# Kernel tuning notes

Measured on AMD Instinct MI355X. Metric: run time of the kernel, lower is better.

The kernel has to match this reference:

```python
import jax, jax.numpy as jnp
import numpy as np

B, M = 32768, 200
NUM_LAYERS, OW, OH = 22, 11, 11
CNN_CH, HIDDEN = 128, 512
ACTION_NVEC = (9, 10)


def setup_inputs() -> dict:
    key = jax.random.key(0)
    ks = jax.random.split(key, 16)
    s = 0.02
    inp = {
        "observations": jax.random.randint(ks[0], (B, M, 3), 0, 256, dtype=jnp.int32),
        "max_vec": jnp.ones((NUM_LAYERS,), dtype=jnp.float32),
        "w_conv1": jax.random.normal(ks[1], (CNN_CH, NUM_LAYERS, 5, 5), jnp.float32) * s,
        "b_conv1": jnp.zeros((CNN_CH,), jnp.float32),
        "w_conv2": jax.random.normal(ks[2], (CNN_CH, CNN_CH, 3, 3), jnp.float32) * s,
        "b_conv2": jnp.zeros((CNN_CH,), jnp.float32),
        "w_fc": jax.random.normal(ks[3], (CNN_CH, HIDDEN // 2), jnp.float32) * s,
        "b_fc": jnp.zeros((HIDDEN // 2,), jnp.float32),
        "w_self": jax.random.normal(ks[4], (NUM_LAYERS, HIDDEN // 2), jnp.float32) * s,
        "b_self": jnp.zeros((HIDDEN // 2,), jnp.float32),
        "w_actor0": jax.random.normal(ks[5], (HIDDEN, ACTION_NVEC[0]), jnp.float32) * 0.01,
        "b_actor0": jnp.zeros((ACTION_NVEC[0],), jnp.float32),
        "w_actor1": jax.random.normal(ks[6], (HIDDEN, ACTION_NVEC[1]), jnp.float32) * 0.01,
        "b_actor1": jnp.zeros((ACTION_NVEC[1],), jnp.float32),
        "w_value": jax.random.normal(ks[7], (HIDDEN, 1), jnp.float32) * s,
        "b_value": jnp.zeros((1,), jnp.float32),
    }
    return inp


def _conv(x, w, b, stride):
    y = jax.lax.conv_general_dilated(
        x, w, window_strides=(stride, stride), padding="VALID",
        dimension_numbers=("NCHW", "OIHW", "NCHW"))
    return y + b[None, :, None, None]


def _encode(observations, max_vec, w_conv1, b_conv1, w_conv2, b_conv2,
            w_fc, b_fc, w_self, b_self):
    # torch: token_observations[token_observations == 255] = 0
    obs = jnp.where(observations == 255, 0, observations)
    coords = obs[..., 0]                       # [B, M]
    x_idx = (coords >> 4) & 15
    y_idx = coords & 15
    atr_idx = obs[..., 1]
    atr_val = obs[..., 2].astype(jnp.float32)
    # coords_byte != 255 is always True after the 255->0 rewrite above
    valid = (x_idx < OW) & (y_idx < OH) & (atr_idx < NUM_LAYERS)
    b_idx = jnp.broadcast_to(jnp.arange(obs.shape[0])[:, None], coords.shape)
    # route invalid tokens to a dummy batch slot B, then drop it
    b_idx = jnp.where(valid, b_idx, obs.shape[0])
    a_idx = jnp.where(valid, atr_idx, 0)
    xs = jnp.where(valid, x_idx, 0)
    ys = jnp.where(valid, y_idx, 0)
    box = jnp.zeros((obs.shape[0] + 1, NUM_LAYERS, OW, OH), jnp.float32)
    box = box.at[b_idx, a_idx, xs, ys].set(atr_val)[: obs.shape[0]]
    features = box / max_vec[None, :, None, None]
    self_feat = jax.nn.relu(features[:, :, 5, 5] @ w_self + b_self)   # [B, 256]
    h = jax.nn.relu(_conv(features, w_conv1, b_conv1, 3))             # [B,128,3,3]
    h = jax.nn.relu(_conv(h, w_conv2, b_conv2, 1))                    # [B,128,1,1]
    h = h.reshape(h.shape[0], -1)                                     # [B,128]
    cnn_feat = jax.nn.relu(h @ w_fc + b_fc)                           # [B,256]
    return jnp.concatenate([self_feat, cnn_feat], axis=1)             # [B,512]


def reference(observations, max_vec, w_conv1, b_conv1, w_conv2, b_conv2,
              w_fc, b_fc, w_self, b_self, w_actor0, b_actor0,
              w_actor1, b_actor1, w_value, b_value):
    hidden = _encode(observations, max_vec, w_conv1, b_conv1, w_conv2, b_conv2,
                     w_fc, b_fc, w_self, b_self)
    logits0 = hidden @ w_actor0 + b_actor0
    logits1 = hidden @ w_actor1 + b_actor1
    value = hidden @ w_value + b_value
    return (logits0, logits1, value, hidden)
```

## Files before the change

kernel.cpp:

```cpp
#include <hip/hip_runtime.h>
#include <hip/hip_bf16.h>

typedef unsigned int uint;
typedef unsigned short ushort;
typedef unsigned long long ull;
typedef __attribute__((ext_vector_type(8))) short short8;
typedef __attribute__((ext_vector_type(4))) float float4_;

#define B_TOT 32768
#define NL    22
#define HID0  ((long)B_TOT * 20)

#define W2F_OFF  0
#define WFCF_OFF 294912
#define WHF_OFF  360448
#define W1T_OFF  393216
#define H1_OFF   674816

__device__ __forceinline__ ushort f2bf(float v) {
  uint x = __float_as_uint(v);
  x += 0x7fffu + ((x >> 16) & 1u);
  return (ushort)(x >> 16);
}

extern "C" __global__ __launch_bounds__(256)
void k_prep(const float* __restrict__ wc1, const float* __restrict__ wc2,
            const float* __restrict__ wfc,
            const float* __restrict__ wa0, const float* __restrict__ wa1,
            const float* __restrict__ wv,
            ushort* __restrict__ w2f, ushort* __restrict__ wfcf,
            ushort* __restrict__ whf, float* __restrict__ w1t)
{
  int i = blockIdx.x * 256 + threadIdx.x;
  if (i < 18432) {
    int l = i & 63, cg = (i >> 6) & 7, ks = i >> 9;
    int col = cg * 16 + (l & 15), kb = ks * 32 + (l >> 4) * 8;
    ushort t[8];
    #pragma unroll
    for (int j = 0; j < 8; ++j) t[j] = f2bf(wc2[col * 1152 + kb + j]);
    uint4 o = { (uint)t[0]|((uint)t[1]<<16), (uint)t[2]|((uint)t[3]<<16),
                (uint)t[4]|((uint)t[5]<<16), (uint)t[6]|((uint)t[7]<<16) };
    ((uint4*)w2f)[i] = o;
  } else if (i < 22528) {
    int i2 = i - 18432;
    int l = i2 & 63, cg = (i2 >> 6) & 15, ks = i2 >> 10;
    int col = cg * 16 + (l & 15), kb = ks * 32 + (l >> 4) * 8;
    ushort t[8];
    #pragma unroll
    for (int j = 0; j < 8; ++j) t[j] = f2bf(wfc[(kb + j) * 256 + col]);
    uint4 o = { (uint)t[0]|((uint)t[1]<<16), (uint)t[2]|((uint)t[3]<<16),
                (uint)t[4]|((uint)t[5]<<16), (uint)t[6]|((uint)t[7]<<16) };
    ((uint4*)wfcf)[i2] = o;
  } else if (i < 24576) {
    int i2 = i - 22528;
    int l = i2 & 63, cg = (i2 >> 6) & 1, ks = i2 >> 7;
    int col = cg * 16 + (l & 15), kb = ks * 32 + (l >> 4) * 8;
    ushort t[8];
    #pragma unroll
    for (int j = 0; j < 8; ++j) {
      int k = kb + j;
      float v = (col < 9)  ? wa0[k*9 + col]
              : (col < 19) ? wa1[k*10 + (col - 9)]
              : (col == 19) ? wv[k] : 0.f;
      t[j] = f2bf(v);
    }
    uint4 o = { (uint)t[0]|((uint)t[1]<<16), (uint)t[2]|((uint)t[3]<<16),
                (uint)t[4]|((uint)t[5]<<16), (uint)t[6]|((uint)t[7]<<16) };
    ((uint4*)whf)[i2] = o;
  } else if (i < 24576 + 70400) {
    int j = i - 24576;
    int oc = j & 127, r = j >> 7;
    w1t[j] = wc1[oc * 550 + r];
  }
}

extern "C" __global__ __launch_bounds__(256)
void k_encode(const int* __restrict__ obs, const float* __restrict__ maxvec,
              const float* __restrict__ w1t, const float* __restrict__ bc1,
              const float* __restrict__ wself, const float* __restrict__ bself,
              float* __restrict__ out, ushort* __restrict__ h1g)
{
  __shared__ uint4  tksf[600];
  __shared__ uint   klist[4][64];
  __shared__ ushort h1su[4][1152];
  __shared__ float  rmaxv[NL];

  const int tid = threadIdx.x, lane = tid & 63, w = tid >> 6;
  const long b = (long)blockIdx.x * 4 + w;

  const uint4* o4 = (const uint4*)obs + (long)blockIdx.x * 600;
  for (int i = tid; i < 600; i += 256) tksf[i] = o4[i];
  if (tid < NL) rmaxv[tid] = 1.0f / maxvec[tid];
  __syncthreads();

  const uint* toks = (const uint*)&tksf[w * 150];
  int cnt = 0;
  #pragma unroll
  for (int r = 0; r < 4; ++r) {
    int m = r * 64 + lane;
    bool valid = false; uint pk = 0;
    if (m < 200) {
      int c = (int)toks[m*3], a = (int)toks[m*3+1], v = (int)toks[m*3+2];
      c = (c == 255) ? 0 : c;  a = (a == 255) ? 0 : a;  v = (v == 255) ? 0 : v;
      int x = (c >> 4) & 15, y = c & 15;
      valid = (x < 11) && (y < 11) && (a < NL);
      pk = ((uint)a << 16) | ((uint)x << 12) | ((uint)y << 8) | (uint)v;
    }
    ull bal = __ballot(valid);
    if (valid) {
      int pos = cnt + __popcll(bal & ((1ull << lane) - 1ull));
      if (pos < 64) klist[w][pos] = pk;
    }
    cnt += __popcll(bal);
  }
  if (cnt > 64) cnt = 64;

  uint u = 0; bool alive = false;
  if (lane < cnt) {
    u = klist[w][lane];
    alive = true;
    uint cell = u >> 8;
    for (int t2 = lane + 1; t2 < cnt; ++t2)
      if ((klist[w][t2] >> 8) == cell) { alive = false; break; }
  }
  ull bal2 = __ballot(alive);
  const int n2 = __popcll(bal2);
  if (alive) {
    int pos = __popcll(bal2 & ((1ull << lane) - 1ull));
    klist[w][pos] = u;
  }
  __syncthreads();

  float a0[9] = {0,0,0,0,0,0,0,0,0}, a1[9] = {0,0,0,0,0,0,0,0,0};
  float s0 = 0.f, s1 = 0.f, s2 = 0.f, s3 = 0.f;
  uint tk = klist[w][0];
  for (int t = 0; t < n2; ++t) {
    uint cur = tk;
    tk = klist[w][(t + 1) & 63];
    int a = cur >> 16, x = (cur >> 12) & 15, y = (cur >> 8) & 15;
    float fv = (float)(cur & 255u) * rmaxv[a];
    if (x == 5 && y == 5) {
      s0 = fmaf(fv, wself[a*256 + lane      ], s0);
      s1 = fmaf(fv, wself[a*256 + 64  + lane], s1);
      s2 = fmaf(fv, wself[a*256 + 128 + lane], s2);
      s3 = fmaf(fv, wself[a*256 + 192 + lane], s3);
    }
    #pragma unroll
    for (int ox = 0; ox < 3; ++ox) {
      int kx = x - 3 * ox;
      if ((unsigned)kx > 4u) continue;
      #pragma unroll
      for (int oy = 0; oy < 3; ++oy) {
        int ky = y - 3 * oy;
        if ((unsigned)ky > 4u) continue;
        const float* wr = w1t + (a*25 + kx*5 + ky) * 128;
        a0[ox*3+oy] = fmaf(fv, wr[lane],      a0[ox*3+oy]);
        a1[ox*3+oy] = fmaf(fv, wr[64 + lane], a1[ox*3+oy]);
      }
    }
  }

  out[HID0 + b*512 + lane      ] = fmaxf(s0 + bself[lane      ], 0.f);
  out[HID0 + b*512 + 64  + lane] = fmaxf(s1 + bself[64  + lane], 0.f);
  out[HID0 + b*512 + 128 + lane] = fmaxf(s2 + bself[128 + lane], 0.f);
  out[HID0 + b*512 + 192 + lane] = fmaxf(s3 + bself[192 + lane], 0.f);

  float bb0 = bc1[lane], bb1 = bc1[64 + lane];
  #pragma unroll
  for (int p = 0; p < 9; ++p) {
    h1su[w][lane*9 + p]        = f2bf(fmaxf(a0[p] + bb0, 0.f));
    h1su[w][(64 + lane)*9 + p] = f2bf(fmaxf(a1[p] + bb1, 0.f));
  }
  const uint* sv = (const uint*)&h1su[w][0];
  const int bbk = (int)(b >> 6), r = (int)(b & 63);
  uint* dstu = (uint*)h1g;
  const long cbase = ((long)bbk * 36) * 64 + r;
  #pragma unroll
  for (int i = lane; i < 576; i += 64) {
    int t = i >> 4;
    dstu[(cbase + (long)t * 64) * 16 + (i & 15)] = sv[i];
  }
}

extern "C" __global__ __launch_bounds__(256)
void k_mlp(const ushort* __restrict__ h1g, const ushort* __restrict__ w2f,
           const float* __restrict__ bc2, const ushort* __restrict__ wfcf,
           const float* __restrict__ bfc, const ushort* __restrict__ whf,
           const float* __restrict__ ba0, const float* __restrict__ ba1,
           const float* __restrict__ bv, float* __restrict__ out)
{
  __shared__ short  Abuf[2][4][64][8];
  __shared__ ushort h2A[16][64][8];

  const int tid = threadIdx.x, lane = tid & 63, w = tid >> 6;
  const int lo = lane & 15, hi = lane >> 4;
  const int bb = blockIdx.x, b0 = bb * 64;

  const short8* w2fv  = (const short8*)w2f;
  const short8* wfcfv = (const short8*)wfcf;
  const uint4*  A4    = (const uint4*)h1g + (long)bb * 36 * 256;

  float4_ acc[4][2];
  #pragma unroll
  for (int cgi = 0; cgi < 2; ++cgi) {
    float bv_ = bc2[(2*w + cgi)*16 + lo];
    float4_ t = {bv_, bv_, bv_, bv_};
    #pragma unroll
    for (int m = 0; m < 4; ++m) acc[m][cgi] = t;
  }

  uint4 rA = A4[tid];
  for (int t = 0; t < 36; ++t) {
    const int cur = t & 1;
    *(uint4*)&Abuf[cur][tid & 3][tid >> 2][0] = rA;
    if (t + 1 < 36) rA = A4[(t + 1) * 256 + tid];
    __syncthreads();
    short8 af[4];
    #pragma unroll
    for (int m = 0; m < 4; ++m)
      af[m] = *(const short8*)&Abuf[cur][hi][m*16 + lo][0];
    #pragma unroll
    for (int cgi = 0; cgi < 2; ++cgi) {
      short8 bf = w2fv[(t*8 + 2*w + cgi)*64 + lane];
      #pragma unroll
      for (int m = 0; m < 4; ++m)
        acc[m][cgi] = __builtin_amdgcn_mfma_f32_16x16x32_bf16(af[m], bf, acc[m][cgi], 0, 0, 0);
    }
  }
  __syncthreads();

  #pragma unroll
  for (int cgi = 0; cgi < 2; ++cgi) {
    int col = (2*w + cgi)*16 + lo;
    #pragma unroll
    for (int m = 0; m < 4; ++m)
      #pragma unroll
      for (int q = 0; q < 4; ++q) {
        int R = m*16 + hi*4 + q;
        h2A[col >> 3][R][col & 7] = f2bf(fmaxf(acc[m][cgi][q], 0.f));
      }
  }
  __syncthreads();

  float4_ acc2[4][4];
  #pragma unroll
  for (int cgi = 0; cgi < 4; ++cgi) {
    float bv_ = bfc[(4*w + cgi)*16 + lo];
    float4_ t = {bv_, bv_, bv_, bv_};
    #pragma unroll
    for (int m = 0; m < 4; ++m) acc2[m][cgi] = t;
  }
  #pragma unroll
  for (int ks = 0; ks < 4; ++ks) {
    short8 af[4];
    #pragma unroll
    for (int m = 0; m < 4; ++m)
      af[m] = *(const short8*)&h2A[ks*4 + hi][m*16 + lo][0];
    #pragma unroll
    for (int cgi = 0; cgi < 4; ++cgi) {
      short8 bf = wfcfv[(ks*16 + 4*w + cgi)*64 + lane];
      #pragma unroll
      for (int m = 0; m < 4; ++m)
        acc2[m][cgi] = __builtin_amdgcn_mfma_f32_16x16x32_bf16(af[m], bf, acc2[m][cgi], 0, 0, 0);
    }
  }

  #pragma unroll
  for (int cgi = 0; cgi < 4; ++cgi) {
    int col = (4*w + cgi)*16 + lo;
    #pragma unroll
    for (int m = 0; m < 4; ++m)
      #pragma unroll
      for (int q = 0; q < 4; ++q) {
        int R = m*16 + hi*4 + q;
        out[HID0 + (long)(b0 + R)*512 + 256 + col] = fmaxf(acc2[m][cgi][q], 0.f);
      }
  }
  __syncthreads();

  const short8* whfv = (const short8*)whf;
  float4_ acc3[2];
  #pragma unroll
  for (int cg = 0; cg < 2; ++cg) {
    int col = cg*16 + lo;
    float bias = (col < 9) ? ba0[col] : (col < 19) ? ba1[col - 9]
               : (col == 19) ? bv[0] : 0.f;
    float4_ t = {bias, bias, bias, bias};
    acc3[cg] = t;
  }

  const float* hrow = out + HID0 + (long)(b0 + w*16 + lo) * 512;
  #pragma unroll
  for (int ks = 0; ks < 16; ++ks) {
    float4_ f0 = *(const float4_*)(hrow + ks*32 + hi*8);
    float4_ f1 = *(const float4_*)(hrow + ks*32 + hi*8 + 4);
    union { short8 s; ushort u[8]; } afu;
    afu.u[0] = f2bf(f0[0]); afu.u[1] = f2bf(f0[1]);
    afu.u[2] = f2bf(f0[2]); afu.u[3] = f2bf(f0[3]);
    afu.u[4] = f2bf(f1[0]); afu.u[5] = f2bf(f1[1]);
    afu.u[6] = f2bf(f1[2]); afu.u[7] = f2bf(f1[3]);
    #pragma unroll
    for (int cg = 0; cg < 2; ++cg) {
      short8 bf = whfv[(ks*2 + cg)*64 + lane];
      acc3[cg] = __builtin_amdgcn_mfma_f32_16x16x32_bf16(afu.s, bf, acc3[cg], 0, 0, 0);
    }
  }

  #pragma unroll
  for (int cg = 0; cg < 2; ++cg) {
    int col = cg*16 + lo;
    #pragma unroll
    for (int q = 0; q < 4; ++q) {
      long R = b0 + w*16 + hi*4 + q;
      float v = acc3[cg][q];
      if (col < 9)        out[R*9 + col] = v;
      else if (col < 19)  out[(long)B_TOT*9 + R*10 + (col - 9)] = v;
      else if (col == 19) out[(long)B_TOT*19 + R] = v;
    }
  }
}

extern "C" void kernel_launch(void* const* d_in, const int* in_sizes, int n_in,
                              void* d_out, int out_size, void* d_ws, size_t ws_size,
                              hipStream_t stream) {
  const int* obs      = (const int*)d_in[0];
  const float* maxvec = (const float*)d_in[1];
  const float* wc1    = (const float*)d_in[2];
  const float* bc1    = (const float*)d_in[3];
  const float* wc2    = (const float*)d_in[4];
  const float* bc2    = (const float*)d_in[5];
  const float* wfc    = (const float*)d_in[6];
  const float* bfc    = (const float*)d_in[7];
  const float* wself  = (const float*)d_in[8];
  const float* bself  = (const float*)d_in[9];
  const float* wa0    = (const float*)d_in[10];
  const float* ba0    = (const float*)d_in[11];
  const float* wa1    = (const float*)d_in[12];
  const float* ba1    = (const float*)d_in[13];
  const float* wv     = (const float*)d_in[14];
  const float* bv     = (const float*)d_in[15];
  float* out          = (float*)d_out;

  char* ws = (char*)d_ws;
  ushort* w2f  = (ushort*)(ws + W2F_OFF);
  ushort* wfcf = (ushort*)(ws + WFCF_OFF);
  ushort* whf  = (ushort*)(ws + WHF_OFF);
  float*  w1t  = (float*)(ws + W1T_OFF);
  ushort* h1g  = (ushort*)(ws + H1_OFF);

  k_prep  <<<dim3(371),      dim3(256), 0, stream>>>(wc1, wc2, wfc, wa0, wa1, wv,
                                                     w2f, wfcf, whf, w1t);
  k_encode<<<dim3(B_TOT/4),  dim3(256), 0, stream>>>(obs, maxvec, w1t, bc1,
                                                     wself, bself, out, h1g);
  k_mlp   <<<dim3(B_TOT/64), dim3(256), 0, stream>>>(h1g, w2f, bc2, wfcf, bfc,
                                                     whf, ba0, ba1, bv, out);
}
```

Before: 108.3 us.

## Restructure encode kernel: direct token loads, shuffle dedup, packed bf16 row-major h1

The encode kernel now reads tokens straight from global memory instead of staging them in LDS. It deduplicates cells with wave shuffles instead of an LDS scan, broadcasts reciprocal max values by shuffle, and drops both block barriers. Weight and bias loads become float2 so each lane owns two adjacent channels, and conv1 outputs are packed with v_cvt_pk_bf16_f32 into a per-sample row-major h1 layout. k_mlp is changed to read that layout with a 144-uint4 row stride. The intent is to cut LDS traffic, barriers and conversion instructions, but the MLP's A-tile loads become strided by rows rather than fully contiguous.

```diff
diff --git a/kernel.cpp b/kernel.cpp
--- a/kernel.cpp
+++ b/kernel.cpp
@@ -21,6 +21,12 @@
   uint x = __float_as_uint(v);
   x += 0x7fffu + ((x >> 16) & 1u);
   return (ushort)(x >> 16);
+}
+
+__device__ __forceinline__ uint cvtpk(float lo, float hi) {
+  uint r;
+  asm volatile("v_cvt_pk_bf16_f32 %0, %1, %2" : "=v"(r) : "v"(lo), "v"(hi));
+  return r;
 }
 
 extern "C" __global__ __launch_bounds__(256)
@@ -80,31 +86,25 @@
               const float* __restrict__ wself, const float* __restrict__ bself,
               float* __restrict__ out, ushort* __restrict__ h1g)
 {
-  __shared__ uint4  tksf[600];
-  __shared__ uint   klist[4][64];
-  __shared__ ushort h1su[4][1152];
-  __shared__ float  rmaxv[NL];
+  __shared__ uint klist[4][64];
 
   const int tid = threadIdx.x, lane = tid & 63, w = tid >> 6;
   const long b = (long)blockIdx.x * 4 + w;
 
-  const uint4* o4 = (const uint4*)obs + (long)blockIdx.x * 600;
-  for (int i = tid; i < 600; i += 256) tksf[i] = o4[i];
-  if (tid < NL) rmaxv[tid] = 1.0f / maxvec[tid];
-  __syncthreads();
-
-  const uint* toks = (const uint*)&tksf[w * 150];
+  float rm_own = (lane < NL) ? (1.0f / maxvec[lane]) : 0.f;
+
+  const uint* ob = (const uint*)obs + b * 600;
   int cnt = 0;
   #pragma unroll
   for (int r = 0; r < 4; ++r) {
     int m = r * 64 + lane;
     bool valid = false; uint pk = 0;
     if (m < 200) {
-      int c = (int)toks[m*3], a = (int)toks[m*3+1], v = (int)toks[m*3+2];
-      c = (c == 255) ? 0 : c;  a = (a == 255) ? 0 : a;  v = (v == 255) ? 0 : v;
-      int x = (c >> 4) & 15, y = c & 15;
-      valid = (x < 11) && (y < 11) && (a < NL);
-      pk = ((uint)a << 16) | ((uint)x << 12) | ((uint)y << 8) | (uint)v;
+      uint c = ob[m*3], a = ob[m*3+1], v = ob[m*3+2];
+      c = (c == 255u) ? 0u : c;  a = (a == 255u) ? 0u : a;  v = (v == 255u) ? 0u : v;
+      uint x = (c >> 4) & 15u, y = c & 15u;
+      valid = (x < 11u) && (y < 11u) && (a < NL);
+      pk = (a << 16) | (x << 12) | (y << 8) | v;
     }
     ull bal = __ballot(valid);
     if (valid) {
@@ -115,35 +115,30 @@
   }
   if (cnt > 64) cnt = 64;
 
-  uint u = 0; bool alive = false;
-  if (lane < cnt) {
-    u = klist[w][lane];
-    alive = true;
-    uint cell = u >> 8;
-    for (int t2 = lane + 1; t2 < cnt; ++t2)
-      if ((klist[w][t2] >> 8) == cell) { alive = false; break; }
+  uint u = (lane < cnt) ? klist[w][lane] : 0xffffffffu;
+  uint cell = u >> 8;
+  bool alive = (lane < cnt);
+  for (int d = 1; d < cnt; ++d) {
+    uint oc_ = __shfl_down(cell, d);
+    alive = alive && !((lane + d < cnt) && (oc_ == cell));
   }
   ull bal2 = __ballot(alive);
   const int n2 = __popcll(bal2);
-  if (alive) {
-    int pos = __popcll(bal2 & ((1ull << lane) - 1ull));
-    klist[w][pos] = u;
-  }
-  __syncthreads();
+  if (alive) klist[w][__popcll(bal2 & ((1ull << lane) - 1ull))] = u;
 
   float a0[9] = {0,0,0,0,0,0,0,0,0}, a1[9] = {0,0,0,0,0,0,0,0,0};
-  float s0 = 0.f, s1 = 0.f, s2 = 0.f, s3 = 0.f;
+  float2 sa = {0.f, 0.f}, sb = {0.f, 0.f};
   uint tk = klist[w][0];
   for (int t = 0; t < n2; ++t) {
     uint cur = tk;
     tk = klist[w][(t + 1) & 63];
     int a = cur >> 16, x = (cur >> 12) & 15, y = (cur >> 8) & 15;
-    float fv = (float)(cur & 255u) * rmaxv[a];
+    float fv = (float)(cur & 255u) * __shfl(rm_own, a);
     if (x == 5 && y == 5) {
-      s0 = fmaf(fv, wself[a*256 + lane      ], s0);
-      s1 = fmaf(fv, wself[a*256 + 64  + lane], s1);
-      s2 = fmaf(fv, wself[a*256 + 128 + lane], s2);
-      s3 = fmaf(fv, wself[a*256 + 192 + lane], s3);
+      const float2* ws2 = (const float2*)(wself + a * 256);
+      float2 w0 = ws2[lane], w1 = ws2[64 + lane];
+      sa.x = fmaf(fv, w0.x, sa.x);  sa.y = fmaf(fv, w0.y, sa.y);
+      sb.x = fmaf(fv, w1.x, sb.x);  sb.y = fmaf(fv, w1.y, sb.y);
     }
     #pragma unroll
     for (int ox = 0; ox < 3; ++ox) {
@@ -153,32 +148,44 @@
       for (int oy = 0; oy < 3; ++oy) {
         int ky = y - 3 * oy;
         if ((unsigned)ky > 4u) continue;
-        const float* wr = w1t + (a*25 + kx*5 + ky) * 128;
-        a0[ox*3+oy] = fmaf(fv, wr[lane],      a0[ox*3+oy]);
-        a1[ox*3+oy] = fmaf(fv, wr[64 + lane], a1[ox*3+oy]);
+        float2 wv2 = ((const float2*)(w1t + (a*25 + kx*5 + ky) * 128))[lane];
+        a0[ox*3+oy] = fmaf(fv, wv2.x, a0[ox*3+oy]);
+        a1[ox*3+oy] = fmaf(fv, wv2.y, a1[ox*3+oy]);
       }
     }
   }
 
-  out[HID0 + b*512 + lane      ] = fmaxf(s0 + bself[lane      ], 0.f);
-  out[HID0 + b*512 + 64  + lane] = fmaxf(s1 + bself[64  + lane], 0.f);
-  out[HID0 + b*512 + 128 + lane] = fmaxf(s2 + bself[128 + lane], 0.f);
-  out[HID0 + b*512 + 192 + lane] = fmaxf(s3 + bself[192 + lane], 0.f);
-
-  float bb0 = bc1[lane], bb1 = bc1[64 + lane];
-  #pragma unroll
-  for (int p = 0; p < 9; ++p) {
-    h1su[w][lane*9 + p]        = f2bf(fmaxf(a0[p] + bb0, 0.f));
-    h1su[w][(64 + lane)*9 + p] = f2bf(fmaxf(a1[p] + bb1, 0.f));
-  }
-  const uint* sv = (const uint*)&h1su[w][0];
-  const int bbk = (int)(b >> 6), r = (int)(b & 63);
-  uint* dstu = (uint*)h1g;
-  const long cbase = ((long)bbk * 36) * 64 + r;
-  #pragma unroll
-  for (int i = lane; i < 576; i += 64) {
-    int t = i >> 4;
-    dstu[(cbase + (long)t * 64) * 16 + (i & 15)] = sv[i];
+  {
+    const float2* bs2 = (const float2*)bself;
+    float2 b0_ = bs2[lane], b1_ = bs2[64 + lane];
+    float2 o0 = { fmaxf(sa.x + b0_.x, 0.f), fmaxf(sa.y + b0_.y, 0.f) };
+    float2 o1 = { fmaxf(sb.x + b1_.x, 0.f), fmaxf(sb.y + b1_.y, 0.f) };
+    float2* out2 = (float2*)(out + HID0 + b * 512);
+    out2[lane] = o0;
+    out2[64 + lane] = o1;
+  }
+
+  {
+    const float2 bc = ((const float2*)bc1)[lane];
+    float v0[9], v1[9];
+    #pragma unroll
+    for (int p = 0; p < 9; ++p) {
+      v0[p] = fmaxf(a0[p] + bc.x, 0.f);
+      v1[p] = fmaxf(a1[p] + bc.y, 0.f);
+    }
+    uint wds[9];
+    wds[0] = cvtpk(v0[0], v0[1]);
+    wds[1] = cvtpk(v0[2], v0[3]);
+    wds[2] = cvtpk(v0[4], v0[5]);
+    wds[3] = cvtpk(v0[6], v0[7]);
+    wds[4] = cvtpk(v0[8], v1[0]);
+    wds[5] = cvtpk(v1[1], v1[2]);
+    wds[6] = cvtpk(v1[3], v1[4]);
+    wds[7] = cvtpk(v1[5], v1[6]);
+    wds[8] = cvtpk(v1[7], v1[8]);
+    uint* dst = (uint*)h1g + b * 576 + 9 * lane;
+    #pragma unroll
+    for (int j = 0; j < 9; ++j) dst[j] = wds[j];
   }
 }
 
@@ -198,7 +205,8 @@
 
   const short8* w2fv  = (const short8*)w2f;
   const short8* wfcfv = (const short8*)wfcf;
-  const uint4*  A4    = (const uint4*)h1g + (long)bb * 36 * 256;
+  const uint4*  A4    = (const uint4*)h1g;
+  const long    arow  = (long)(b0 + (tid >> 2)) * 144 + (tid & 3);
 
   float4_ acc[4][2];
   #pragma unroll
@@ -209,11 +217,11 @@
     for (int m = 0; m < 4; ++m) acc[m][cgi] = t;
   }
 
-  uint4 rA = A4[tid];
+  uint4 rA = A4[arow];
   for (int t = 0; t < 36; ++t) {
     const int cur = t & 1;
     *(uint4*)&Abuf[cur][tid & 3][tid >> 2][0] = rA;
-    if (t + 1 < 36) rA = A4[(t + 1) * 256 + tid];
+    if (t + 1 < 36) rA = A4[arow + (t + 1) * 4];
     __syncthreads();
     short8 af[4];
     #pragma unroll
```

Measured after the change: 109.5 us. Within noise of the previous version (+1.1%).
